# Performance work log

Measured on AMD Instinct MI355X. Metric: run time of the kernel, lower is better.

Reference implementation:

```python
import jax, jax.numpy as jnp
import numpy as np

N = 50000
E = 800000
NODE_IN = 16
EDGE_IN = 8
HID = 128
OUT = 128
HEADS = 4
HC = HID // HEADS          # per-head channels = 32
EH = HID // 2              # edge hidden = 64
EPS = 1e-5
NEG_SLOPE = 0.2            # PyG GATConv leaky_relu slope


def setup_inputs() -> dict:
    key = jax.random.key(0)
    ks = list(jax.random.split(key, 16))
    it = iter(ks)
    nx = lambda: next(it)
    s = 0.05
    p = {}
    p["x"] = jax.random.normal(nx(), (N, NODE_IN), jnp.float32)
    p["edge_index"] = jax.random.randint(nx(), (2, E), 0, N)
    p["edge_attr"] = jax.random.normal(nx(), (E, EDGE_IN), jnp.float32)
    # node_preprocess: Linear + LayerNorm
    p["np_w"] = jax.random.normal(nx(), (NODE_IN, HID), jnp.float32) * s
    p["np_b"] = jnp.zeros((HID,), jnp.float32)
    p["np_g"] = jnp.ones((HID,), jnp.float32)
    p["np_be"] = jnp.zeros((HID,), jnp.float32)
    # edge_preprocess: Linear + LayerNorm
    p["ep_w"] = jax.random.normal(nx(), (EDGE_IN, EH), jnp.float32) * s
    p["ep_b"] = jnp.zeros((EH,), jnp.float32)
    p["ep_g"] = jnp.ones((EH,), jnp.float32)
    p["ep_be"] = jnp.zeros((EH,), jnp.float32)
    # 3 stacked GATConv layers (params stacked on leading dim)
    p["gat_w"] = jax.random.normal(nx(), (3, HID, HID), jnp.float32) * s
    p["gat_as"] = jax.random.normal(nx(), (3, HEADS, HC), jnp.float32) * s
    p["gat_ad"] = jax.random.normal(nx(), (3, HEADS, HC), jnp.float32) * s
    p["gat_ew"] = jax.random.normal(nx(), (3, EH, HID), jnp.float32) * s
    p["gat_ae"] = jax.random.normal(nx(), (3, HEADS, HC), jnp.float32) * s
    p["gat_b"] = jnp.zeros((3, HID), jnp.float32)
    # BatchNorm affine params
    p["bn_g"] = jnp.ones((3, HID), jnp.float32)
    p["bn_b"] = jnp.zeros((3, HID), jnp.float32)
    # final_proj: Linear + LayerNorm
    p["fp_w"] = jax.random.normal(nx(), (HID, OUT), jnp.float32) * s
    p["fp_b"] = jnp.zeros((OUT,), jnp.float32)
    p["fp_g"] = jnp.ones((OUT,), jnp.float32)
    p["fp_be"] = jnp.zeros((OUT,), jnp.float32)
    return p


def _ln(x, g, b):
    m = x.mean(-1, keepdims=True)
    v = ((x - m) ** 2).mean(-1, keepdims=True)
    return (x - m) * jax.lax.rsqrt(v + EPS) * g + b


def _bn(x, g, b):  # training-mode batch statistics over node dim
    m = x.mean(0)
    v = ((x - m) ** 2).mean(0)
    return (x - m) * jax.lax.rsqrt(v + EPS) * g + b


def _gat(h, e, src, dst, W, a_s, a_d, We, a_e, bias):
    # h: [N, HID], e: [E2, EH], src/dst: [E2]
    xs = (h @ W).reshape(N, HEADS, HC)                       # [N,H,C]
    al_s = (xs * a_s).sum(-1)                                # [N,H]
    al_d = (xs * a_d).sum(-1)                                # [N,H]
    eh = (e @ We).reshape(-1, HEADS, HC)                     # [E2,H,C]
    alpha = al_s[src] + al_d[dst] + (eh * a_e).sum(-1)       # [E2,H]
    alpha = jnp.where(alpha >= 0, alpha, NEG_SLOPE * alpha)  # leaky relu
    # segment softmax over incoming edges of each dst node
    amax = jax.ops.segment_max(alpha, dst, num_segments=N)
    ex = jnp.exp(alpha - amax[dst])
    w = ex / jax.ops.segment_sum(ex, dst, num_segments=N)[dst]
    msg = xs[src] * w[:, :, None]                            # [E2,H,C]
    out = jax.ops.segment_sum(msg, dst, num_segments=N)      # [N,H,C]
    return out.reshape(N, HID) + bias


def reference(x, edge_index, edge_attr, np_w, np_b, np_g, np_be,
              ep_w, ep_b, ep_g, ep_be,
              gat_w, gat_as, gat_ad, gat_ew, gat_ae, gat_b,
              bn_g, bn_b, fp_w, fp_b, fp_g, fp_be):
    src, dst = edge_index[0], edge_index[1]
    h = jax.nn.relu(_ln(x @ np_w + np_b, np_g, np_be))
    e = jax.nn.relu(_ln(edge_attr @ ep_w + ep_b, ep_g, ep_be))
    # PyG GATConv default add_self_loops=True, fill_value='mean':
    # self-loop edge_attr = mean of incoming edge_attr per dst node (0 if none)
    deg = jax.ops.segment_sum(jnp.ones((E,), e.dtype), dst, num_segments=N)
    loop_e = jax.ops.segment_sum(e, dst, num_segments=N) / jnp.maximum(deg, 1.0)[:, None]
    ar = jnp.arange(N)
    src2 = jnp.concatenate([src, ar])
    dst2 = jnp.concatenate([dst, ar])
    e2 = jnp.concatenate([e, loop_e], axis=0)
    for i in range(3):
        res = h
        h = _gat(h, e2, src2, dst2, gat_w[i], gat_as[i], gat_ad[i],
                 gat_ew[i], gat_ae[i], gat_b[i])
        h = jax.nn.relu(_bn(h, bn_g[i], bn_b[i]) + res)
    return _ln(h @ fp_w + fp_b, fp_g, fp_be)
```

## Files before the change

kernel.cpp:

```cpp
#include <hip/hip_runtime.h>
#include <hip/hip_bf16.h>
#include <math.h>

#define N_NODES 50000
#define N_EDGES 800000
#define EPS 1e-5f
#define SLOPE 0.2f

typedef unsigned int u32;
typedef unsigned short u16;
typedef float floatx4 __attribute__((ext_vector_type(4)));
typedef short short8_t __attribute__((ext_vector_type(8)));

__device__ __forceinline__ float bf2f(u16 v) {
    u32 u = ((u32)v) << 16;
    return __uint_as_float(u);
}
__device__ __forceinline__ u16 f2bf(float f) {
    u32 u = __float_as_uint(f);
    u32 r = (u + 0x7fffu + ((u >> 16) & 1u)) >> 16;
    return (u16)r;
}
__device__ __forceinline__ float lo_bf(u32 v) { return __uint_as_float(v << 16); }
__device__ __forceinline__ float hi_bf(u32 v) { return __uint_as_float(v & 0xffff0000u); }
__device__ __forceinline__ float wred(float v) {
    #pragma unroll
    for (int off = 32; off > 0; off >>= 1) v += __shfl_xor(v, off, 64);
    return v;
}

__global__ void k_M(const float* __restrict__ ew, const float* __restrict__ ae,
                    float* __restrict__ M) {
    int t = threadIdx.x;
    if (t >= 768) return;
    int k = t / 12, j = t % 12;
    int l = j >> 2, h = j & 3;
    const float* ewp = ew + l * 8192 + k * 128 + h * 32;
    const float* aep = ae + l * 128 + h * 32;
    float s = 0.f;
    #pragma unroll
    for (int c = 0; c < 32; c++) s += ewp[c] * aep[c];
    M[k * 12 + j] = s;
}

__global__ void k_convW(const float* __restrict__ w, u16* __restrict__ hi,
                        u16* __restrict__ lo) {
    int i = blockIdx.x * 256 + threadIdx.x;
    if (i >= 3 * 128 * 128) return;
    int l = i >> 14, r = i & 16383;
    int n = r >> 7, k = r & 127;
    float f = w[(size_t)l * 16384 + k * 128 + n];
    u16 hb = f2bf(f);
    hi[i] = hb;
    lo[i] = f2bf(f - bf2f(hb));
}

__global__ __launch_bounds__(256) void k_node_pre(
        const float* __restrict__ x, const float* __restrict__ w,
        const float* __restrict__ b, const float* __restrict__ g,
        const float* __restrict__ be, float* __restrict__ h) {
    int wave = threadIdx.x >> 6, lane = threadIdx.x & 63;
    int n = blockIdx.x * 4 + wave;
    if (n >= N_NODES) return;
    const float* xr = x + (size_t)n * 16;
    float xv[16];
    #pragma unroll
    for (int k = 0; k < 16; k++) xv[k] = xr[k];
    int c0 = lane, c1 = lane + 64;
    float a0 = b[c0], a1 = b[c1];
    #pragma unroll
    for (int k = 0; k < 16; k++) {
        a0 = fmaf(xv[k], w[k * 128 + c0], a0);
        a1 = fmaf(xv[k], w[k * 128 + c1], a1);
    }
    float m = wred(a0 + a1) * (1.f / 128.f);
    float d0 = a0 - m, d1 = a1 - m;
    float v = wred(d0 * d0 + d1 * d1) * (1.f / 128.f);
    float rs = rsqrtf(v + EPS);
    float o0 = d0 * rs * g[c0] + be[c0];
    float o1 = d1 * rs * g[c1] + be[c1];
    h[(size_t)n * 128 + c0] = fmaxf(o0, 0.f);
    h[(size_t)n * 128 + c1] = fmaxf(o1, 0.f);
}

__global__ void k_deg(const int* __restrict__ dst, int* __restrict__ deg) {
    int e = blockIdx.x * 256 + threadIdx.x;
    if (e < N_EDGES) atomicAdd(&deg[dst[e]], 1);
}

__global__ void k_scan1(const int* __restrict__ deg, int* __restrict__ incl,
                        int* __restrict__ bsum) {
    __shared__ int lds[1024];
    int i = blockIdx.x * 1024 + threadIdx.x;
    int v = (i < N_NODES) ? deg[i] : 0;
    lds[threadIdx.x] = v;
    __syncthreads();
    for (int off = 1; off < 1024; off <<= 1) {
        int t = (threadIdx.x >= off) ? lds[threadIdx.x - off] : 0;
        __syncthreads();
        lds[threadIdx.x] += t;
        __syncthreads();
    }
    if (i < N_NODES) incl[i] = lds[threadIdx.x];
    if (threadIdx.x == 1023) bsum[blockIdx.x] = lds[1023];
}
__global__ void k_scan2(int* __restrict__ bsum, int nb) {
    if (threadIdx.x == 0 && blockIdx.x == 0) {
        int run = 0;
        for (int i = 0; i < nb; i++) { int t = bsum[i]; bsum[i] = run; run += t; }
    }
}
__global__ void k_scan3(const int* __restrict__ incl, const int* __restrict__ bsum,
                        int* __restrict__ rowptr) {
    int i = blockIdx.x * 1024 + threadIdx.x;
    if (i < N_NODES) rowptr[i + 1] = incl[i] + bsum[blockIdx.x];
    if (i == 0) rowptr[0] = 0;
}

__global__ __launch_bounds__(256) void k_edge(
        const int* __restrict__ ei, const float* __restrict__ ea,
        const float* __restrict__ epw, const float* __restrict__ epb,
        const float* __restrict__ epg, const float* __restrict__ epbe,
        const float* __restrict__ M, const int* __restrict__ rowptr,
        int* __restrict__ cursor, int* __restrict__ csr_src,
        float* __restrict__ csr_aE) {
    __shared__ float sW[512], sM[768], sB[64], sG[64], sBe[64];
    for (int i = threadIdx.x; i < 512; i += 256) sW[i] = epw[i];
    for (int i = threadIdx.x; i < 768; i += 256) sM[i] = M[i];
    if (threadIdx.x < 64) {
        sB[threadIdx.x] = epb[threadIdx.x];
        sG[threadIdx.x] = epg[threadIdx.x];
        sBe[threadIdx.x] = epbe[threadIdx.x];
    }
    __syncthreads();
    int e = blockIdx.x * 256 + threadIdx.x;
    if (e >= N_EDGES) return;
    int src = ei[e], dst = ei[N_EDGES + e];
    float xa[8];
    #pragma unroll
    for (int k = 0; k < 8; k++) xa[k] = ea[(size_t)e * 8 + k];
    float v[64];
    float sum = 0.f;
    #pragma unroll
    for (int c = 0; c < 64; c++) {
        float a = sB[c];
        #pragma unroll
        for (int k = 0; k < 8; k++) a = fmaf(xa[k], sW[k * 64 + c], a);
        v[c] = a; sum += a;
    }
    float m = sum * (1.f / 64.f);
    float var = 0.f;
    #pragma unroll
    for (int c = 0; c < 64; c++) { float d = v[c] - m; var += d * d; }
    float rs = rsqrtf(var * (1.f / 64.f) + EPS);
    #pragma unroll
    for (int c = 0; c < 64; c++) {
        float o = (v[c] - m) * rs * sG[c] + sBe[c];
        v[c] = fmaxf(o, 0.f);
    }
    float aE[12];
    #pragma unroll
    for (int j = 0; j < 12; j++) aE[j] = 0.f;
    #pragma unroll
    for (int c = 0; c < 64; c++) {
        float vc = v[c];
        #pragma unroll
        for (int j = 0; j < 12; j++) aE[j] = fmaf(vc, sM[c * 12 + j], aE[j]);
    }
    int slot = rowptr[dst] + atomicAdd(&cursor[dst], 1);
    csr_src[slot] = src;
    #pragma unroll
    for (int l = 0; l < 3; l++) {
        float4 w4;
        w4.x = aE[l * 4 + 0]; w4.y = aE[l * 4 + 1];
        w4.z = aE[l * 4 + 2]; w4.w = aE[l * 4 + 3];
        *(float4*)(csr_aE + ((size_t)l * N_EDGES + slot) * 4) = w4;
    }
}

__global__ __launch_bounds__(256) void k_gemm_xs_mfma(
        const float* __restrict__ h, const u16* __restrict__ wt_hi,
        const u16* __restrict__ wt_lo, u16* __restrict__ xs) {
    int wave = threadIdx.x >> 6, lane = threadIdx.x & 63;
    int r0 = (blockIdx.x * 4 + wave) * 16;
    if (r0 >= N_NODES) return;
    int lrow = lane & 15, lk = lane >> 4;
    const float* ap = h + (size_t)(r0 + lrow) * 128 + lk * 8;
    const u16* bph = wt_hi + lrow * 128 + lk * 8;
    const u16* bpl = wt_lo + lrow * 128 + lk * 8;
    floatx4 acc[8];
    #pragma unroll
    for (int j = 0; j < 8; j++) acc[j] = (floatx4){0.f, 0.f, 0.f, 0.f};
    #pragma unroll
    for (int s = 0; s < 4; s++) {
        float4 v0 = *(const float4*)(ap + s * 32);
        float4 v1 = *(const float4*)(ap + s * 32 + 4);
        float av[8] = {v0.x, v0.y, v0.z, v0.w, v1.x, v1.y, v1.z, v1.w};
        short8_t ahi, alo;
        #pragma unroll
        for (int i = 0; i < 8; i++) {
            u16 hb = f2bf(av[i]);
            ahi[i] = (short)hb;
            alo[i] = (short)f2bf(av[i] - bf2f(hb));
        }
        short8_t bh[8], bl[8];
        #pragma unroll
        for (int j = 0; j < 8; j++) {
            bh[j] = *(const short8_t*)(bph + s * 32 + j * 2048);
            bl[j] = *(const short8_t*)(bpl + s * 32 + j * 2048);
        }
        #pragma unroll
        for (int j = 0; j < 8; j++)
            acc[j] = __builtin_amdgcn_mfma_f32_16x16x32_bf16(ahi, bh[j], acc[j], 0, 0, 0);
        #pragma unroll
        for (int j = 0; j < 8; j++)
            acc[j] = __builtin_amdgcn_mfma_f32_16x16x32_bf16(ahi, bl[j], acc[j], 0, 0, 0);
        #pragma unroll
        for (int j = 0; j < 8; j++)
            acc[j] = __builtin_amdgcn_mfma_f32_16x16x32_bf16(alo, bh[j], acc[j], 0, 0, 0);
    }
    u16* orow = xs + (size_t)(r0 + lk * 4) * 128 + lrow;
    #pragma unroll
    for (int j = 0; j < 8; j++) {
        #pragma unroll
        for (int reg = 0; reg < 4; reg++)
            orow[(size_t)reg * 128 + j * 16] = f2bf(acc[j][reg]);
    }
}

__global__ void k_al(const u16* __restrict__ xs, const float* __restrict__ as_,
                     const float* __restrict__ ad_, float* __restrict__ al_s,
                     float* __restrict__ al_d) {
    int t = blockIdx.x * 256 + threadIdx.x;
    if (t >= N_NODES * 4) return;
    int n = t >> 2, hh = t & 3;
    const uint4* xp = (const uint4*)(xs + (size_t)n * 128 + hh * 32);
    const float* app = as_ + hh * 32;
    const float* dpp = ad_ + hh * 32;
    float s = 0.f, d = 0.f;
    #pragma unroll
    for (int q = 0; q < 4; q++) {
        uint4 v = xp[q];
        u32 wv[4] = {v.x, v.y, v.z, v.w};
        #pragma unroll
        for (int p = 0; p < 4; p++) {
            int c = q * 8 + p * 2;
            float fl = lo_bf(wv[p]), fh = hi_bf(wv[p]);
            s = fmaf(fl, app[c], s); s = fmaf(fh, app[c + 1], s);
            d = fmaf(fl, dpp[c], d); d = fmaf(fh, dpp[c + 1], d);
        }
    }
    al_s[t] = s; al_d[t] = d;
}

__global__ __launch_bounds__(256) void k_agg(
        const int* __restrict__ rowptr, const int* __restrict__ csr_src,
        const float* __restrict__ aEl, const float* __restrict__ al_s,
        const float* __restrict__ al_d, const u16* __restrict__ xs,
        const float* __restrict__ bias, float* __restrict__ outp) {
    int lane = threadIdx.x & 63;
    int n = __builtin_amdgcn_readfirstlane(blockIdx.x * 4 + (threadIdx.x >> 6));
    if (n >= N_NODES) return;
    int row = rowptr[n], end = rowptr[n + 1];
    int hh = lane >> 4;
    const u32* xsw = (const u32*)xs;
    float ald = al_d[n * 4 + hh];
    float asn = al_s[n * 4 + hh];
    u32 xnp = xsw[(size_t)n * 64 + lane];
    float acc0 = 0.f, acc1 = 0.f, ssum = 0.f, aes = 0.f;
    int slot = row;
    for (; slot + 4 <= end; slot += 4) {
        int sA = csr_src[slot],     sB = csr_src[slot + 1];
        int sC = csr_src[slot + 2], sD = csr_src[slot + 3];
        const float* aep = aEl + (size_t)slot * 4 + hh;
        float aeA = aep[0], aeB = aep[4], aeC = aep[8], aeD = aep[12];
        float asA = al_s[sA * 4 + hh], asB = al_s[sB * 4 + hh];
        float asC = al_s[sC * 4 + hh], asD = al_s[sD * 4 + hh];
        u32 xA = xsw[(size_t)sA * 64 + lane], xB = xsw[(size_t)sB * 64 + lane];
        u32 xC = xsw[(size_t)sC * 64 + lane], xD = xsw[(size_t)sD * 64 + lane];
        aes += (aeA + aeB) + (aeC + aeD);
        float aA = asA + ald + aeA; aA = (aA >= 0.f) ? aA : SLOPE * aA;
        float aB = asB + ald + aeB; aB = (aB >= 0.f) ? aB : SLOPE * aB;
        float aC = asC + ald + aeC; aC = (aC >= 0.f) ? aC : SLOPE * aC;
        float aD = asD + ald + aeD; aD = (aD >= 0.f) ? aD : SLOPE * aD;
        float eA = __expf(aA), eB = __expf(aB), eC = __expf(aC), eD = __expf(aD);
        ssum += (eA + eB) + (eC + eD);
        acc0 = fmaf(eA, lo_bf(xA), acc0); acc1 = fmaf(eA, hi_bf(xA), acc1);
        acc0 = fmaf(eB, lo_bf(xB), acc0); acc1 = fmaf(eB, hi_bf(xB), acc1);
        acc0 = fmaf(eC, lo_bf(xC), acc0); acc1 = fmaf(eC, hi_bf(xC), acc1);
        acc0 = fmaf(eD, lo_bf(xD), acc0); acc1 = fmaf(eD, hi_bf(xD), acc1);
    }
    for (; slot < end; slot++) {
        int sA = csr_src[slot];
        float aeA = aEl[(size_t)slot * 4 + hh];
        float asA = al_s[sA * 4 + hh];
        u32 xA = xsw[(size_t)sA * 64 + lane];
        aes += aeA;
        float aA = asA + ald + aeA; aA = (aA >= 0.f) ? aA : SLOPE * aA;
        float eA = __expf(aA);
        ssum += eA;
        acc0 = fmaf(eA, lo_bf(xA), acc0); acc1 = fmaf(eA, hi_bf(xA), acc1);
    }
    float dinv = 1.f / fmaxf((float)(end - row), 1.f);
    float sa = asn + ald + aes * dinv; sa = (sa >= 0.f) ? sa : SLOPE * sa;
    float e = __expf(sa);
    ssum += e;
    acc0 = fmaf(e, lo_bf(xnp), acc0); acc1 = fmaf(e, hi_bf(xnp), acc1);
    float2 bv = *(const float2*)(bias + lane * 2);
    float2 o;
    o.x = acc0 / ssum + bv.x;
    o.y = acc1 / ssum + bv.y;
    *(float2*)(outp + (size_t)n * 128 + lane * 2) = o;
}

__global__ void k_bn_stats(const float* __restrict__ x, float* __restrict__ stats) {
    __shared__ float lds[512];
    int t = threadIdx.x;
    int c = t & 127, half = t >> 7;
    float s = 0.f, q = 0.f;
    for (int n = blockIdx.x * 2 + half; n < N_NODES; n += gridDim.x * 2) {
        float v = x[(size_t)n * 128 + c];
        s += v; q = fmaf(v, v, q);
    }
    lds[t] = s; lds[256 + t] = q;
    __syncthreads();
    if (t < 128) {
        atomicAdd(&stats[c], lds[t] + lds[t + 128]);
        atomicAdd(&stats[128 + c], lds[256 + t] + lds[256 + t + 128]);
    }
}

__global__ void k_bn_apply(const float* __restrict__ outp, const float* __restrict__ stats,
                           const float* __restrict__ g, const float* __restrict__ b,
                           float* __restrict__ h) {
    int idx = blockIdx.x * 256 + threadIdx.x;
    if (idx >= N_NODES * 128) return;
    int c = idx & 127;
    float m = stats[c] * (1.f / N_NODES);
    float var = stats[128 + c] * (1.f / N_NODES) - m * m;
    float rs = rsqrtf(var + EPS);
    float v = (outp[idx] - m) * rs * g[c] + b[c] + h[idx];
    h[idx] = fmaxf(v, 0.f);
}

__global__ __launch_bounds__(256) void k_gemm_fp(
        const float* __restrict__ h, const float* __restrict__ W,
        const float* __restrict__ fb, const float* __restrict__ g,
        const float* __restrict__ be, float* __restrict__ out) {
    __shared__ float2 sW[64 * 64];
    __shared__ float sH[16][128];
    int tid = threadIdx.x;
    int base = blockIdx.x * 16;
    for (int i = tid; i < 2048; i += 256) {
        int r = i >> 7, c = i & 127;
        int n = base + r;
        sH[r][c] = (n < N_NODES) ? h[(size_t)n * 128 + c] : 0.f;
    }
    int wave = tid >> 6, lane = tid & 63;
    float acc[4][2];
    #pragma unroll
    for (int r = 0; r < 4; r++) { acc[r][0] = 0.f; acc[r][1] = 0.f; }
    for (int half = 0; half < 2; half++) {
        __syncthreads();
        for (int i = tid; i < 4096; i += 256) {
            int k = (i >> 6) + half * 64, j = i & 63;
            sW[i] = make_float2(W[k * 128 + j], W[k * 128 + j + 64]);
        }
        __syncthreads();
        #pragma unroll 8
        for (int k2 = 0; k2 < 64; k2++) {
            float2 wv = sW[k2 * 64 + lane];
            int k = half * 64 + k2;
            #pragma unroll
            for (int r = 0; r < 4; r++) {
                float hk = sH[wave * 4 + r][k];
                acc[r][0] = fmaf(hk, wv.x, acc[r][0]);
                acc[r][1] = fmaf(hk, wv.y, acc[r][1]);
            }
        }
    }
    #pragma unroll
    for (int r = 0; r < 4; r++) {
        int n = base + wave * 4 + r;
        float y0 = acc[r][0] + fb[lane];
        float y1 = acc[r][1] + fb[lane + 64];
        float m = wred(y0 + y1) * (1.f / 128.f);
        float d0 = y0 - m, d1 = y1 - m;
        float var = wred(d0 * d0 + d1 * d1) * (1.f / 128.f);
        float rs = rsqrtf(var + EPS);
        if (n < N_NODES) {
            out[(size_t)n * 128 + lane]      = d0 * rs * g[lane] + be[lane];
            out[(size_t)n * 128 + lane + 64] = d1 * rs * g[lane + 64] + be[lane + 64];
        }
    }
}

extern "C" void kernel_launch(void* const* d_in, const int* in_sizes, int n_in,
                              void* d_out, int out_size, void* d_ws, size_t ws_size,
                              hipStream_t stream) {
    const float* x      = (const float*)d_in[0];
    const int*   ei     = (const int*)d_in[1];
    const float* ea     = (const float*)d_in[2];
    const float* np_w   = (const float*)d_in[3];
    const float* np_b   = (const float*)d_in[4];
    const float* np_g   = (const float*)d_in[5];
    const float* np_be  = (const float*)d_in[6];
    const float* ep_w   = (const float*)d_in[7];
    const float* ep_b   = (const float*)d_in[8];
    const float* ep_g   = (const float*)d_in[9];
    const float* ep_be  = (const float*)d_in[10];
    const float* gat_w  = (const float*)d_in[11];
    const float* gat_as = (const float*)d_in[12];
    const float* gat_ad = (const float*)d_in[13];
    const float* gat_ew = (const float*)d_in[14];
    const float* gat_ae = (const float*)d_in[15];
    const float* gat_b  = (const float*)d_in[16];
    const float* bn_g   = (const float*)d_in[17];
    const float* bn_b   = (const float*)d_in[18];
    const float* fp_w   = (const float*)d_in[19];
    const float* fp_b   = (const float*)d_in[20];
    const float* fp_g   = (const float*)d_in[21];
    const float* fp_be  = (const float*)d_in[22];
    float* out = (float*)d_out;

    char* ws = (char*)d_ws;
    size_t off = 0;
    auto alloc = [&](size_t bytes) -> void* {
        void* p = ws + off;
        off = (off + bytes + 255) & ~(size_t)255;
        return p;
    };
    float* h      = (float*)alloc((size_t)N_NODES * 128 * 4);
    float* buf    = (float*)alloc((size_t)N_NODES * 128 * 4);
    u16*   xs     = (u16*)alloc((size_t)N_NODES * 128 * 2);
    float* al_s   = (float*)alloc((size_t)N_NODES * 4 * 4);
    float* al_d   = (float*)alloc((size_t)N_NODES * 4 * 4);
    int*   deg    = (int*)alloc((size_t)N_NODES * 4);
    int*   rowptr = (int*)alloc((size_t)(N_NODES + 1) * 4);
    int*   cursor = (int*)alloc((size_t)N_NODES * 4);
    int*   incl   = (int*)alloc((size_t)N_NODES * 4);
    int*   bsum   = (int*)alloc(64 * 4);
    int*   csr_src= (int*)alloc((size_t)N_EDGES * 4);
    float* csr_aE = (float*)alloc((size_t)N_EDGES * 12 * 4);
    float* M      = (float*)alloc(64 * 12 * 4);
    float* stats  = (float*)alloc(256 * 4);
    u16*   wt_hi  = (u16*)alloc((size_t)3 * 16384 * 2);
    u16*   wt_lo  = (u16*)alloc((size_t)3 * 16384 * 2);

    hipMemsetAsync(deg, 0, (size_t)N_NODES * 4, stream);
    hipMemsetAsync(cursor, 0, (size_t)N_NODES * 4, stream);

    k_M<<<1, 768, 0, stream>>>(gat_ew, gat_ae, M);
    k_convW<<<192, 256, 0, stream>>>(gat_w, wt_hi, wt_lo);
    k_node_pre<<<(N_NODES + 3) / 4, 256, 0, stream>>>(x, np_w, np_b, np_g, np_be, h);
    k_deg<<<(N_EDGES + 255) / 256, 256, 0, stream>>>(ei + N_EDGES, deg);
    int nblk = (N_NODES + 1023) / 1024;
    k_scan1<<<nblk, 1024, 0, stream>>>(deg, incl, bsum);
    k_scan2<<<1, 64, 0, stream>>>(bsum, nblk);
    k_scan3<<<nblk, 1024, 0, stream>>>(incl, bsum, rowptr);
    k_edge<<<(N_EDGES + 255) / 256, 256, 0, stream>>>(ei, ea, ep_w, ep_b, ep_g, ep_be,
                                                      M, rowptr, cursor, csr_src, csr_aE);

    for (int l = 0; l < 3; l++) {
        k_gemm_xs_mfma<<<(3125 + 3) / 4, 256, 0, stream>>>(
            h, wt_hi + (size_t)l * 16384, wt_lo + (size_t)l * 16384, xs);
        k_al<<<(N_NODES * 4 + 255) / 256, 256, 0, stream>>>(xs, gat_as + l * 128,
                                                            gat_ad + l * 128, al_s, al_d);
        hipMemsetAsync(stats, 0, 256 * 4, stream);
        k_agg<<<(N_NODES + 3) / 4, 256, 0, stream>>>(rowptr, csr_src,
                                                     csr_aE + (size_t)l * N_EDGES * 4,
                                                     al_s, al_d, xs, gat_b + l * 128, buf);
        k_bn_stats<<<256, 256, 0, stream>>>(buf, stats);
        k_bn_apply<<<(N_NODES * 128 + 255) / 256, 256, 0, stream>>>(buf, stats,
                                                                    bn_g + l * 128,
                                                                    bn_b + l * 128, h);
    }
    k_gemm_fp<<<(N_NODES + 15) / 16, 256, 0, stream>>>(h, fp_w, fp_b, fp_g, fp_be, out);
}
```

Baseline: 743.4 us.

## Split edge CSR fill from edge MLP, unroll aggregation by 8, vectorize BN apply

After: 731.4 us. No clear change (-1.6%).

```diff
diff --git a/kernel.cpp b/kernel.cpp
--- a/kernel.cpp
+++ b/kernel.cpp
@@ -117,12 +117,20 @@
     if (i == 0) rowptr[0] = 0;
 }
 
-__global__ __launch_bounds__(256) void k_edge(
-        const int* __restrict__ ei, const float* __restrict__ ea,
+__global__ void k_fill(const int* __restrict__ ei, const int* __restrict__ rowptr,
+                       int* __restrict__ cursor, int2* __restrict__ csr_se) {
+    int e = blockIdx.x * 256 + threadIdx.x;
+    if (e >= N_EDGES) return;
+    int src = ei[e], dst = ei[N_EDGES + e];
+    int slot = rowptr[dst] + atomicAdd(&cursor[dst], 1);
+    csr_se[slot] = make_int2(src, e);
+}
+
+__global__ __launch_bounds__(256) void k_edge_c(
+        const int2* __restrict__ csr_se, const float* __restrict__ ea,
         const float* __restrict__ epw, const float* __restrict__ epb,
         const float* __restrict__ epg, const float* __restrict__ epbe,
-        const float* __restrict__ M, const int* __restrict__ rowptr,
-        int* __restrict__ cursor, int* __restrict__ csr_src,
+        const float* __restrict__ M, int* __restrict__ csr_src,
         float* __restrict__ csr_aE) {
     __shared__ float sW[512], sM[768], sB[64], sG[64], sBe[64];
     for (int i = threadIdx.x; i < 512; i += 256) sW[i] = epw[i];
@@ -133,12 +141,13 @@
         sBe[threadIdx.x] = epbe[threadIdx.x];
     }
     __syncthreads();
-    int e = blockIdx.x * 256 + threadIdx.x;
-    if (e >= N_EDGES) return;
-    int src = ei[e], dst = ei[N_EDGES + e];
-    float xa[8];
-    #pragma unroll
-    for (int k = 0; k < 8; k++) xa[k] = ea[(size_t)e * 8 + k];
+    int s = blockIdx.x * 256 + threadIdx.x;
+    if (s >= N_EDGES) return;
+    int2 se = csr_se[s];
+    int src = se.x, e = se.y;
+    float4 x0 = *(const float4*)(ea + (size_t)e * 8);
+    float4 x1 = *(const float4*)(ea + (size_t)e * 8 + 4);
+    float xa[8] = {x0.x, x0.y, x0.z, x0.w, x1.x, x1.y, x1.z, x1.w};
     float v[64];
     float sum = 0.f;
     #pragma unroll
@@ -167,14 +176,13 @@
         #pragma unroll
         for (int j = 0; j < 12; j++) aE[j] = fmaf(vc, sM[c * 12 + j], aE[j]);
     }
-    int slot = rowptr[dst] + atomicAdd(&cursor[dst], 1);
-    csr_src[slot] = src;
+    csr_src[s] = src;
     #pragma unroll
     for (int l = 0; l < 3; l++) {
         float4 w4;
         w4.x = aE[l * 4 + 0]; w4.y = aE[l * 4 + 1];
         w4.z = aE[l * 4 + 2]; w4.w = aE[l * 4 + 3];
-        *(float4*)(csr_aE + ((size_t)l * N_EDGES + slot) * 4) = w4;
+        *(float4*)(csr_aE + ((size_t)l * N_EDGES + s) * 4) = w4;
     }
 }
 
@@ -269,26 +277,45 @@
     u32 xnp = xsw[(size_t)n * 64 + lane];
     float acc0 = 0.f, acc1 = 0.f, ssum = 0.f, aes = 0.f;
     int slot = row;
+    for (; slot + 8 <= end; slot += 8) {
+        int sv[8]; float ae[8], asv[8]; u32 xv[8];
+        #pragma unroll
+        for (int i = 0; i < 8; i++) sv[i] = csr_src[slot + i];
+        #pragma unroll
+        for (int i = 0; i < 8; i++) ae[i] = aEl[(size_t)(slot + i) * 4 + hh];
+        #pragma unroll
+        for (int i = 0; i < 8; i++) asv[i] = al_s[sv[i] * 4 + hh];
+        #pragma unroll
+        for (int i = 0; i < 8; i++) xv[i] = xsw[(size_t)sv[i] * 64 + lane];
+        #pragma unroll
+        for (int i = 0; i < 8; i++) {
+            aes += ae[i];
+            float a = asv[i] + ald + ae[i]; a = (a >= 0.f) ? a : SLOPE * a;
+            float ev = __expf(a);
+            ssum += ev;
+            acc0 = fmaf(ev, lo_bf(xv[i]), acc0);
+            acc1 = fmaf(ev, hi_bf(xv[i]), acc1);
+        }
+    }
     for (; slot + 4 <= end; slot += 4) {
-        int sA = csr_src[slot],     sB = csr_src[slot + 1];
-        int sC = csr_src[slot + 2], sD = csr_src[slot + 3];
-        const float* aep = aEl + (size_t)slot * 4 + hh;
-        float aeA = aep[0], aeB = aep[4], aeC = aep[8], aeD = aep[12];
-        float asA = al_s[sA * 4 + hh], asB = al_s[sB * 4 + hh];
-        float asC = al_s[sC * 4 + hh], asD = al_s[sD * 4 + hh];
-        u32 xA = xsw[(size_t)sA * 64 + lane], xB = xsw[(size_t)sB * 64 + lane];
-        u32 xC = xsw[(size_t)sC * 64 + lane], xD = xsw[(size_t)sD * 64 + lane];
-        aes += (aeA + aeB) + (aeC + aeD);
-        float aA = asA + ald + aeA; aA = (aA >= 0.f) ? aA : SLOPE * aA;
-        float aB = asB + ald + aeB; aB = (aB >= 0.f) ? aB : SLOPE * aB;
-        float aC = asC + ald + aeC; aC = (aC >= 0.f) ? aC : SLOPE * aC;
-        float aD = asD + ald + aeD; aD = (aD >= 0.f) ? aD : SLOPE * aD;
-        float eA = __expf(aA), eB = __expf(aB), eC = __expf(aC), eD = __expf(aD);
-        ssum += (eA + eB) + (eC + eD);
-        acc0 = fmaf(eA, lo_bf(xA), acc0); acc1 = fmaf(eA, hi_bf(xA), acc1);
-        acc0 = fmaf(eB, lo_bf(xB), acc0); acc1 = fmaf(eB, hi_bf(xB), acc1);
-        acc0 = fmaf(eC, lo_bf(xC), acc0); acc1 = fmaf(eC, hi_bf(xC), acc1);
-        acc0 = fmaf(eD, lo_bf(xD), acc0); acc1 = fmaf(eD, hi_bf(xD), acc1);
+        int sv[4]; float ae[4], asv[4]; u32 xv[4];
+        #pragma unroll
+        for (int i = 0; i < 4; i++) sv[i] = csr_src[slot + i];
+        #pragma unroll
+        for (int i = 0; i < 4; i++) ae[i] = aEl[(size_t)(slot + i) * 4 + hh];
+        #pragma unroll
+        for (int i = 0; i < 4; i++) asv[i] = al_s[sv[i] * 4 + hh];
+        #pragma unroll
+        for (int i = 0; i < 4; i++) xv[i] = xsw[(size_t)sv[i] * 64 + lane];
+        #pragma unroll
+        for (int i = 0; i < 4; i++) {
+            aes += ae[i];
+            float a = asv[i] + ald + ae[i]; a = (a >= 0.f) ? a : SLOPE * a;
+            float ev = __expf(a);
+            ssum += ev;
+            acc0 = fmaf(ev, lo_bf(xv[i]), acc0);
+            acc1 = fmaf(ev, hi_bf(xv[i]), acc1);
+        }
     }
     for (; slot < end; slot++) {
         int sA = csr_src[slot];
@@ -330,17 +357,23 @@
     }
 }
 
-__global__ void k_bn_apply(const float* __restrict__ outp, const float* __restrict__ stats,
+__global__ void k_bn_apply(const floatx4* __restrict__ outp, const float* __restrict__ stats,
                            const float* __restrict__ g, const float* __restrict__ b,
-                           float* __restrict__ h) {
+                           floatx4* __restrict__ h) {
     int idx = blockIdx.x * 256 + threadIdx.x;
-    if (idx >= N_NODES * 128) return;
-    int c = idx & 127;
-    float m = stats[c] * (1.f / N_NODES);
-    float var = stats[128 + c] * (1.f / N_NODES) - m * m;
-    float rs = rsqrtf(var + EPS);
-    float v = (outp[idx] - m) * rs * g[c] + b[c] + h[idx];
-    h[idx] = fmaxf(v, 0.f);
+    if (idx >= N_NODES * 32) return;
+    int c0 = (idx & 31) * 4;
+    floatx4 o = outp[idx], hv = h[idx], r;
+    #pragma unroll
+    for (int p = 0; p < 4; p++) {
+        int c = c0 + p;
+        float m = stats[c] * (1.f / N_NODES);
+        float var = stats[128 + c] * (1.f / N_NODES) - m * m;
+        float rs = rsqrtf(var + EPS);
+        float v = (o[p] - m) * rs * g[c] + b[c] + hv[p];
+        r[p] = fmaxf(v, 0.f);
+    }
+    h[idx] = r;
 }
 
 __global__ __launch_bounds__(256) void k_gemm_fp(
@@ -446,6 +479,7 @@
     float* stats  = (float*)alloc(256 * 4);
     u16*   wt_hi  = (u16*)alloc((size_t)3 * 16384 * 2);
     u16*   wt_lo  = (u16*)alloc((size_t)3 * 16384 * 2);
+    int2*  csr_se = (int2*)buf;
 
     hipMemsetAsync(deg, 0, (size_t)N_NODES * 4, stream);
     hipMemsetAsync(cursor, 0, (size_t)N_NODES * 4, stream);
@@ -458,8 +492,9 @@
     k_scan1<<<nblk, 1024, 0, stream>>>(deg, incl, bsum);
     k_scan2<<<1, 64, 0, stream>>>(bsum, nblk);
     k_scan3<<<nblk, 1024, 0, stream>>>(incl, bsum, rowptr);
-    k_edge<<<(N_EDGES + 255) / 256, 256, 0, stream>>>(ei, ea, ep_w, ep_b, ep_g, ep_be,
-                                                      M, rowptr, cursor, csr_src, csr_aE);
+    k_fill<<<(N_EDGES + 255) / 256, 256, 0, stream>>>(ei, rowptr, cursor, csr_se);
+    k_edge_c<<<(N_EDGES + 255) / 256, 256, 0, stream>>>(csr_se, ea, ep_w, ep_b, ep_g,
+                                                        ep_be, M, csr_src, csr_aE);
 
     for (int l = 0; l < 3; l++) {
         k_gemm_xs_mfma<<<(3125 + 3) / 4, 256, 0, stream>>>(
@@ -471,9 +506,8 @@
                                                      csr_aE + (size_t)l * N_EDGES * 4,
                                                      al_s, al_d, xs, gat_b + l * 128, buf);
         k_bn_stats<<<256, 256, 0, stream>>>(buf, stats);
-        k_bn_apply<<<(N_NODES * 128 + 255) / 256, 256, 0, stream>>>(buf, stats,
-                                                                    bn_g + l * 128,
-                                                                    bn_b + l * 128, h);
+        k_bn_apply<<<(N_NODES * 32 + 255) / 256, 256, 0, stream>>>(
+            (const floatx4*)buf, stats, bn_g + l * 128, bn_b + l * 128, (floatx4*)h);
     }
     k_gemm_fp<<<(N_NODES + 15) / 16, 256, 0, stream>>>(h, fp_w, fp_b, fp_g, fp_be, out);
 }
```
